# Kernel tuning notes

Hardware: AMD Instinct MI355X
Metric: run time of the kernel (lower is better)

Reference implementation:

```python
import jax, jax.numpy as jnp
import numpy as np

D = 4096       # hidden_size
H = 32         # n_heads (tp_size=1)
DN = 128       # qk_nope_head_dim
DR = 64        # qk_rope_head_dim
DV = 128       # v_head_dim
QL = 1536      # q_lora_rank
KL = 512       # kv_lora_rank
S = 2048       # seqlen, start_pos = 0
EPS = 1e-6
SCALE = (DN + DR) ** -0.5  # softmax_scale (no yarn mscale: seqlen <= original_seq_len)
THETA = 10000.0


def _freqs(seqlen, dim, base=THETA):
    # precompute_freqs_cis without yarn correction (seqlen <= original_seq_len)
    inv = 1.0 / (base ** (np.arange(0, dim, 2, dtype=np.float32) / dim))
    f = np.outer(np.arange(seqlen, dtype=np.float32), inv)  # [S, dim//2]
    return jnp.asarray(np.cos(f)), jnp.asarray(np.sin(f))


def _rmsnorm(x, w):
    return x * jax.lax.rsqrt(jnp.mean(x * x, axis=-1, keepdims=True) + EPS) * w


def _rope(x, cos, sin):
    # x: [S, H, R]; complex rotation on consecutive pairs (view_as_complex semantics)
    S_, H_, R_ = x.shape
    xr = x.reshape(S_, H_, R_ // 2, 2)
    x0, x1 = xr[..., 0], xr[..., 1]
    c = cos[:, None, :]
    s = sin[:, None, :]
    y0 = x0 * c - x1 * s
    y1 = x0 * s + x1 * c
    return jnp.stack([y0, y1], axis=-1).reshape(S_, H_, R_)


def setup_inputs() -> dict:
    key = jax.random.key(0)
    ks = jax.random.split(key, 6)
    std = 0.02
    return {
        "x": jax.random.normal(ks[0], (S, D), jnp.float32),
        "wq_a": jax.random.normal(ks[1], (QL, D), jnp.float32) * std,
        "q_norm_w": jnp.ones((QL,), jnp.float32),
        "wq_b": jax.random.normal(ks[2], (H * (DN + DR), QL), jnp.float32) * std,
        "wkv_a": jax.random.normal(ks[3], (KL + DR, D), jnp.float32) * std,
        "kv_norm_w": jnp.ones((KL,), jnp.float32),
        "wkv_b": jax.random.normal(ks[4], (H * (DN + DV), KL), jnp.float32) * std,
        "wo": jax.random.normal(ks[5], (D, H * DV), jnp.float32) * std,
    }


def reference(x, wq_a, q_norm_w, wq_b, wkv_a, kv_norm_w, wkv_b, wo):
    cos, sin = _freqs(S, DR)

    # q path: low-rank down-proj + RMSNorm + up-proj
    q = _rmsnorm(x @ wq_a.T, q_norm_w) @ wq_b.T          # [S, H*(DN+DR)]
    q = q.reshape(S, H, DN + DR)
    q_nope, q_pe = q[..., :DN], q[..., DN:]
    q_pe = _rope(q_pe, cos, sin)                          # [S, H, DR]

    # kv path: joint latent + rope part
    kv_all = x @ wkv_a.T                                  # [S, KL+DR]
    kv = _rmsnorm(kv_all[:, :KL], kv_norm_w)              # latent kv cache [S, KL]
    k_pe = _rope(kv_all[:, None, KL:], cos, sin)[:, 0, :]  # pe cache [S, DR]

    # absorb k-up-projection into q (einsum 'shd,hdc->shc')
    wkv_b_r = wkv_b.reshape(H, DN + DV, KL)
    q_lat = jnp.einsum("shd,hdc->shc", q_nope, wkv_b_r[:, :DN])  # [S, H, KL]

    scores = (jnp.einsum("shc,tc->sht", q_lat, kv)
              + jnp.einsum("shr,tr->sht", q_pe, k_pe)) * SCALE   # [S, H, T]

    causal = jnp.arange(S)[:, None] >= jnp.arange(S)[None, :]     # [S, T]
    scores = jnp.where(causal[:, None, :], scores, -jnp.inf)
    p = jax.nn.softmax(scores, axis=-1)

    o_lat = jnp.einsum("sht,tc->shc", p, kv)                      # [S, H, KL]
    o = jnp.einsum("shc,hdc->shd", o_lat, wkv_b_r[:, DN:])        # [S, H, DV]
    return o.reshape(S, H * DV) @ wo.T                            # [S, D]
```

## Files before the change

### kernel.cpp

```cpp
#include <hip/hip_runtime.h>
#include <hip/hip_bf16.h>
#include <type_traits>

using bf16 = __hip_bfloat16;
typedef short v8s __attribute__((ext_vector_type(8)));
typedef float v4f __attribute__((ext_vector_type(4)));

#define DEV __device__ __forceinline__

constexpr float SCALE_ = 0.07216878364870322f;

DEV unsigned short bfu(float f) {
  bf16 h = __float2bfloat16(f);
  return __builtin_bit_cast(unsigned short, h);
}
DEV float b2f(short u) {
  unsigned int x = ((unsigned int)(unsigned short)u) << 16;
  return __builtin_bit_cast(float, x);
}

DEV void g2lds16(const void* g, void* l) {
  __builtin_amdgcn_global_load_lds(
      (const __attribute__((address_space(1))) unsigned int*)g,
      (__attribute__((address_space(3))) unsigned int*)l, 16, 0, 0);
}


__global__ void cast_kernel(const float* __restrict__ in, bf16* __restrict__ out, int n4) {
  int i = blockIdx.x * 256 + threadIdx.x;
  int stride = gridDim.x * 256;
  for (; i < n4; i += stride) {
    float4 v = ((const float4*)in)[i];
    ushort4 u;
    u.x = bfu(v.x); u.y = bfu(v.y); u.z = bfu(v.z); u.w = bfu(v.w);
    ((ushort4*)out)[i] = u;
  }
}

__global__ void cast_pad_kernel(const float* __restrict__ in, bf16* __restrict__ out) {
  int i = blockIdx.x * 256 + threadIdx.x;
  float4 v = make_float4(0.f, 0.f, 0.f, 0.f);
  if (i < 589824) v = ((const float4*)in)[i];
  ushort4 u;
  u.x = bfu(v.x); u.y = bfu(v.y); u.z = bfu(v.z); u.w = bfu(v.w);
  ((ushort4*)out)[i] = u;
}

__global__ void wkvbt_kernel(const float* __restrict__ wkvb, bf16* __restrict__ out) {
  int gid = blockIdx.x * 256 + threadIdx.x;
  int c8 = (gid & 63) * 8;
  int d8 = ((gid >> 6) & 15) * 8;
  int h = gid >> 10;
  float4 a[8][2];
#pragma unroll
  for (int r = 0; r < 8; ++r) {
    const float* p = wkvb + ((long)(h * 256 + d8 + r)) * 512 + c8;
    a[r][0] = *(const float4*)p;
    a[r][1] = *(const float4*)(p + 4);
  }
#pragma unroll
  for (int cc = 0; cc < 8; ++cc) {
    v8s o;
#pragma unroll
    for (int r = 0; r < 8; ++r) {
      float f = (cc < 4) ? ((const float*)&a[r][0])[cc] : ((const float*)&a[r][1])[cc - 4];
      o[r] = (short)bfu(f);
    }
    *(v8s*)(out + (long)h * 65536 + (c8 + cc) * 128 + d8) = o;
  }
}

__global__ void wkvbv_kernel(const float* __restrict__ wkvb, bf16* __restrict__ out) {
  int i = blockIdx.x * 256 + threadIdx.x;
  int c4 = i & 127, d = (i >> 7) & 127, h = i >> 14;
  float4 v = *(const float4*)(wkvb + ((long)(h * 256 + 128 + d)) * 512 + c4 * 4);
  ushort4 u;
  u.x = bfu(v.x); u.y = bfu(v.y); u.z = bfu(v.z); u.w = bfu(v.w);
  *(ushort4*)(out + ((long)(h * 128 + d)) * 512 + c4 * 4) = u;
}

__global__ void freqs_kernel(float* __restrict__ cosb, float* __restrict__ sinb) {
  int t = blockIdx.x * 256 + threadIdx.x;
  int s = t >> 5, i = t & 31;
  float inv = powf(10000.0f, -(float)(2 * i) / 64.0f);
  float f = (float)s * inv;
  cosb[t] = cosf(f);
  sinb[t] = sinf(f);
}

__global__ void rmsnorm_bf_kernel(const bf16* __restrict__ in, const float* __restrict__ w,
                                  bf16* __restrict__ out, int L, int ldin, int ldout) {
  int row = blockIdx.x;
  const bf16* x = in + (long)row * ldin;
  int L8 = L >> 3;
  float ss = 0.f;
  for (int i = threadIdx.x; i < L8; i += 256) {
    v8s v = *(const v8s*)(x + i * 8);
#pragma unroll
    for (int j = 0; j < 8; ++j) { float f = b2f(v[j]); ss += f * f; }
  }
#pragma unroll
  for (int d = 1; d < 64; d <<= 1) ss += __shfl_xor(ss, d);
  __shared__ float red[4];
  if ((threadIdx.x & 63) == 0) red[threadIdx.x >> 6] = ss;
  __syncthreads();
  float r = rsqrtf((red[0] + red[1] + red[2] + red[3]) / (float)L + 1e-6f);
  bf16* o = out + (long)row * ldout;
  for (int i = threadIdx.x; i < L8; i += 256) {
    v8s v = *(const v8s*)(x + i * 8);
    v8s u;
#pragma unroll
    for (int j = 0; j < 8; ++j)
      u[j] = (short)bfu(b2f(v[j]) * r * w[i * 8 + j]);
    *(v8s*)(o + i * 8) = u;
  }
}

__global__ void rope_kpe_kernel(const bf16* __restrict__ kvall, const float* __restrict__ cosb,
                                const float* __restrict__ sinb, bf16* __restrict__ keff) {
  int t = blockIdx.x * 256 + threadIdx.x;
  int s = t >> 5, i = t & 31;
  const bf16* p = kvall + (long)s * 640 + 512;
  float x0 = __bfloat162float(p[2 * i]), x1 = __bfloat162float(p[2 * i + 1]);
  float c = cosb[t], sn = sinb[t];
  bf16* o = keff + (long)s * 576 + 512;
  o[2 * i] = __float2bfloat16(x0 * c - x1 * sn);
  o[2 * i + 1] = __float2bfloat16(x0 * sn + x1 * c);
}

__global__ void rope_q_kernel(const bf16* __restrict__ qf, const float* __restrict__ cosb,
                              const float* __restrict__ sinb, bf16* __restrict__ qeff) {
  int t = blockIdx.x * 256 + threadIdx.x;
  int i = t & 31, h = (t >> 5) & 31, s = t >> 10;
  const bf16* p = qf + (long)s * 6144 + h * 192 + 128;
  float x0 = __bfloat162float(p[2 * i]), x1 = __bfloat162float(p[2 * i + 1]);
  float c = cosb[s * 32 + i], sn = sinb[s * 32 + i];
  bf16* o = qeff + (long)s * 18432 + h * 576 + 512;
  o[2 * i] = __float2bfloat16(x0 * c - x1 * sn);
  o[2 * i + 1] = __float2bfloat16(x0 * sn + x1 * c);
}

__global__ void vtrans_kernel(const bf16* __restrict__ keff, bf16* __restrict__ vT) {
  int gid = blockIdx.x * 256 + threadIdx.x;
  int t8 = (gid & 255) * 8, c8 = (gid >> 8) * 8;
  v8s in[8];
#pragma unroll
  for (int r = 0; r < 8; ++r)
    in[r] = *(const v8s*)(keff + (long)(t8 + r) * 576 + c8);
#pragma unroll
  for (int cc = 0; cc < 8; ++cc) {
    v8s o;
#pragma unroll
    for (int r = 0; r < 8; ++r) o[r] = in[r][cc];
    *(v8s*)(vT + (long)(c8 + cc) * 2048 + t8) = o;
  }
}

template <typename OutT>
__global__ __launch_bounds__(256, 3) void gemm_bt(
    const bf16* __restrict__ A, const bf16* __restrict__ B, OutT* __restrict__ C,
    int K, int lda, int ldb, int ldc, long sA, long sB, long sC) {
  __shared__ bf16 lA[4096];
  __shared__ bf16 lB[4096];
  const int tid = threadIdx.x;
  const int lane = tid & 63;
  const int w = tid >> 6, wm = w >> 1, wn = w & 1;
  const int r16 = lane & 15, kg = (lane >> 4) << 3;
  const int arow = tid >> 2, acol = (tid & 3) << 3;
  const bf16* Ab = A + (long)blockIdx.z * sA + (long)blockIdx.y * 128 * lda;
  const bf16* Bb = B + (long)blockIdx.z * sB + (long)blockIdx.x * 128 * ldb;
  v4f acc[4][4] = {};
  for (int k0 = 0; k0 < K; k0 += 32) {
    __syncthreads();
#pragma unroll
    for (int i = 0; i < 2; ++i) {
      g2lds16(Ab + (long)(i * 64 + arow) * lda + (k0 + acol), &lA[i * 2048 + w * 512]);
      g2lds16(Bb + (long)(i * 64 + arow) * ldb + (k0 + acol), &lB[i * 2048 + w * 512]);
    }
    __syncthreads();
    v8s af[4], bfr[4];
#pragma unroll
    for (int mi = 0; mi < 4; ++mi)
      af[mi] = *(const v8s*)&lA[(wm * 64 + mi * 16 + r16) * 32 + kg];
#pragma unroll
    for (int ni = 0; ni < 4; ++ni)
      bfr[ni] = *(const v8s*)&lB[(wn * 64 + ni * 16 + r16) * 32 + kg];
    __builtin_amdgcn_s_setprio(1);
#pragma unroll
    for (int mi = 0; mi < 4; ++mi)
#pragma unroll
      for (int ni = 0; ni < 4; ++ni)
        acc[mi][ni] = __builtin_amdgcn_mfma_f32_16x16x32_bf16(af[mi], bfr[ni], acc[mi][ni], 0, 0, 0);
    __builtin_amdgcn_s_setprio(0);
  }
  OutT* Cb = C + (long)blockIdx.z * sC + (long)(blockIdx.y * 128) * ldc + blockIdx.x * 128;
  const int cr = (lane >> 4) << 2;
#pragma unroll
  for (int mi = 0; mi < 4; ++mi)
#pragma unroll
    for (int ni = 0; ni < 4; ++ni)
#pragma unroll
      for (int j = 0; j < 4; ++j) {
        long idx = (long)(wm * 64 + mi * 16 + cr + j) * ldc + wn * 64 + ni * 16 + r16;
        float v = acc[mi][ni][j];
        if constexpr (std::is_same<OutT, float>::value) Cb[idx] = v;
        else Cb[idx] = __float2bfloat16(v);
      }
}

__device__ const signed char U_QT[24] = {15,15,7,14,14,13,13,6,12,12,11,11,5,10,10,9,9,4,8,8,3,2,1,0};
__device__ const signed char U_HF[24] = {0,1,-1,0,1,0,1,-1,0,1,0,1,-1,0,1,0,1,-1,0,1,-1,-1,-1,-1};

__global__ __launch_bounds__(512, 2) void attn_kernel(
    const bf16* __restrict__ qeff, const bf16* __restrict__ keff,
    const bf16* __restrict__ vT, bf16* __restrict__ olat,
    bf16* __restrict__ P1, float* __restrict__ mlb) {
  __shared__ __align__(16) bf16 kl[32 * 576];
  __shared__ __align__(16) bf16 vl[512 * 32];
  const int tid = threadIdx.x, lane = tid & 63, w = tid >> 6;
  const int r16 = lane & 15, hi = lane >> 4;
  const int kg = hi << 3, cr = hi << 2;
  const int h = blockIdx.x;
  const int u = blockIdx.y;
  const int qt = U_QT[u];
  const int hf = U_HF[u];
  const int nch = 4 * qt + 4;
  const int kc0 = (hf == 1) ? (nch >> 1) : 0;
  const int kc1 = (hf == 0) ? (nch >> 1) : nch;
  const int qrow = qt * 128 + w * 16 + r16;
  const int rb = r16 & 7;

  const long qbase = (long)qrow * 18432 + h * 576;
  v8s qreg[18];
#pragma unroll
  for (int kk = 0; kk < 18; ++kk)
    qreg[kk] = __builtin_nontemporal_load((const v8s*)(qeff + qbase + kk * 32 + kg));

  v4f acc[32] = {};
  float mrow = -1e30f, lrow = 0.f;

  auto stageK = [&](int t0) {
#pragma unroll
    for (int it = 0; it < 5; ++it) {
      int D = it * 512 + tid;
      if (D < 2304) {
        int row = D / 72;
        int gg = D - row * 72;
        int gs = gg ^ (row & 7);
        g2lds16(keff + (long)(t0 + row) * 576 + gs * 8,
                (char*)kl + (it * 512 + w * 64) * 16);
      }
    }
  };
  auto stageV = [&](int t0) {
#pragma unroll
    for (int it = 0; it < 4; ++it) {
      int D = it * 512 + tid;
      int row = D >> 2;
      int s = (D & 3) ^ ((row >> 1) & 3);
      g2lds16(vT + (long)row * 2048 + t0 + s * 8,
              (char*)vl + (it * 512 + w * 64) * 16);
    }
  };

  stageK(kc0 * 32);
  __syncthreads();

  for (int kc = kc0; kc < kc1; ++kc) {
    const int t0 = kc * 32;
    stageV(t0);

    const char* kb = (const char*)kl;
    v4f sf0 = {}, sf1 = {};
    __builtin_amdgcn_s_setprio(1);
#pragma unroll
    for (int kk = 0; kk < 18; ++kk) {
      int so = ((kk * 4 + hi) ^ rb) << 4;
      v8s b0 = *(const v8s*)(kb + r16 * 1152 + so);
      v8s b1 = *(const v8s*)(kb + (16 + r16) * 1152 + so);
      sf0 = __builtin_amdgcn_mfma_f32_16x16x32_bf16(b0, qreg[kk], sf0, 0, 0, 0);
      sf1 = __builtin_amdgcn_mfma_f32_16x16x32_bf16(b1, qreg[kk], sf1, 0, 0, 0);
    }
    __builtin_amdgcn_s_setprio(0);
    float s0[4], s1[4];
#pragma unroll
    for (int j = 0; j < 4; ++j) { s0[j] = sf0[j] * SCALE_; s1[j] = sf1[j] * SCALE_; }
    if (kc >= 4 * qt) {
#pragma unroll
      for (int j = 0; j < 4; ++j) {
        if (t0 + cr + j > qrow) s0[j] = -1e30f;
        if (t0 + 16 + cr + j > qrow) s1[j] = -1e30f;
      }
    }
    float mx = fmaxf(fmaxf(fmaxf(s0[0], s0[1]), fmaxf(s0[2], s0[3])),
                     fmaxf(fmaxf(s1[0], s1[1]), fmaxf(s1[2], s1[3])));
    mx = fmaxf(mx, __shfl_xor(mx, 16));
    mx = fmaxf(mx, __shfl_xor(mx, 32));
    if (!__all(mx <= mrow + 8.0f)) {
      float mn = fmaxf(mrow, mx);
      float alpha = __expf(mrow - mn);
      mrow = mn;
      lrow *= alpha;
      float af0 = __shfl(alpha, cr + 0), af1 = __shfl(alpha, cr + 1);
      float af2 = __shfl(alpha, cr + 2), af3 = __shfl(alpha, cr + 3);
#pragma unroll
      for (int c = 0; c < 32; ++c) {
        acc[c][0] *= af0; acc[c][1] *= af1; acc[c][2] *= af2; acc[c][3] *= af3;
      }
    }
    float p0[4], p1[4];
#pragma unroll
    for (int j = 0; j < 4; ++j) {
      p0[j] = __expf(s0[j] - mrow);
      p1[j] = __expf(s1[j] - mrow);
    }
    float rs = (p0[0] + p0[1]) + (p0[2] + p0[3]) + (p1[0] + p1[1]) + (p1[2] + p1[3]);
    rs += __shfl_xor(rs, 16);
    rs += __shfl_xor(rs, 32);
    lrow += rs;
    int u0 = (int)((unsigned)bfu(p0[0]) | ((unsigned)bfu(p0[1]) << 16));
    int u1 = (int)((unsigned)bfu(p0[2]) | ((unsigned)bfu(p0[3]) << 16));
    int v0 = (int)((unsigned)bfu(p1[0]) | ((unsigned)bfu(p1[1]) << 16));
    int v1 = (int)((unsigned)bfu(p1[2]) | ((unsigned)bfu(p1[3]) << 16));
    const int L1 = r16 + 32 * (hi & 1);
    const int L2 = L1 + 16;
    const bool lo = hi < 2;
    int d0a = __shfl(u0, L1), d0b = __shfl(v0, L1);
    int d1a = __shfl(u1, L1), d1b = __shfl(v1, L1);
    int d2a = __shfl(u0, L2), d2b = __shfl(v0, L2);
    int d3a = __shfl(u1, L2), d3b = __shfl(v1, L2);
    int4 pw = make_int4(lo ? d0a : d0b, lo ? d1a : d1b, lo ? d2a : d2b, lo ? d3a : d3b);
    v8s ap = __builtin_bit_cast(v8s, pw);

    __syncthreads();
    if (kc + 1 < kc1) stageK(t0 + 32);

    __builtin_amdgcn_s_setprio(1);
#pragma unroll
    for (int c = 0; c < 32; ++c) {
      const int vrow = c * 16 + r16;
      const int vsw = (hi ^ ((vrow >> 1) & 3)) << 4;
      v8s bv = *(const v8s*)((const char*)vl + vrow * 64 + vsw);
      acc[c] = __builtin_amdgcn_mfma_f32_16x16x32_bf16(ap, bv, acc[c], 0, 0, 0);
    }
    __builtin_amdgcn_s_setprio(0);
    __syncthreads();
  }
  if (hf < 0) {
    float linv0 = 1.0f / __shfl(lrow, cr + 0);
    float linv1 = 1.0f / __shfl(lrow, cr + 1);
    float linv2 = 1.0f / __shfl(lrow, cr + 2);
    float linv3 = 1.0f / __shfl(lrow, cr + 3);
    const long ob = (long)(qt * 128 + w * 16 + cr) * 16384 + h * 512 + r16;
#pragma unroll
    for (int c = 0; c < 32; ++c) {
      olat[ob + 0 * 16384 + c * 16] = __float2bfloat16(acc[c][0] * linv0);
      olat[ob + 1 * 16384 + c * 16] = __float2bfloat16(acc[c][1] * linv1);
      olat[ob + 2 * 16384 + c * 16] = __float2bfloat16(acc[c][2] * linv2);
      olat[ob + 3 * 16384 + c * 16] = __float2bfloat16(acc[c][3] * linv3);
    }
  } else {
    if (hi == 0) {
      float* mr = mlb + (((qrow - 1024) << 5) + h) * 4 + hf * 2;
      mr[0] = mrow;
      mr[1] = lrow;
    }
    bf16* dst = (hf == 0) ? olat : P1;
    const int rbase = (hf == 0) ? (qt * 128) : (qt * 128 - 1024);
    const long ob = (long)(rbase + w * 16 + cr) * 16384 + h * 512 + r16;
#pragma unroll
    for (int c = 0; c < 32; ++c) {
      dst[ob + 0 * 16384 + c * 16] = __float2bfloat16(acc[c][0]);
      dst[ob + 1 * 16384 + c * 16] = __float2bfloat16(acc[c][1]);
      dst[ob + 2 * 16384 + c * 16] = __float2bfloat16(acc[c][2]);
      dst[ob + 3 * 16384 + c * 16] = __float2bfloat16(acc[c][3]);
    }
  }
}

__global__ void combine_kernel(bf16* __restrict__ olat, const bf16* __restrict__ P1,
                               const float* __restrict__ mlb) {
  int gid = blockIdx.x * 256 + threadIdx.x;
  int cg = gid & 63, h = (gid >> 6) & 31, r = gid >> 11;
  const float* m4 = mlb + ((r << 5) + h) * 4;
  float mA = m4[0], lA = m4[1], mB = m4[2], lB = m4[3];
  float m = fmaxf(mA, mB);
  float sA = __expf(mA - m), sB = __expf(mB - m);
  float inv = 1.0f / (sA * lA + sB * lB);
  sA *= inv; sB *= inv;
  long oa = (long)(1024 + r) * 16384 + h * 512 + cg * 8;
  long ob = (long)r * 16384 + h * 512 + cg * 8;
  v8s a = *(const v8s*)(olat + oa);
  v8s b = *(const v8s*)(P1 + ob);
  v8s o;
#pragma unroll
  for (int j = 0; j < 8; ++j)
    o[j] = (short)bfu(b2f(a[j]) * sA + b2f(b[j]) * sB);
  *(v8s*)(olat + oa) = o;
}


extern "C" void kernel_launch(void* const* d_in, const int* in_sizes, int n_in,
                              void* d_out, int out_size, void* d_ws, size_t ws_size,
                              hipStream_t stream) {
  const float* x = (const float*)d_in[0];
  const float* wq_a = (const float*)d_in[1];
  const float* q_norm_w = (const float*)d_in[2];
  const float* wq_b = (const float*)d_in[3];
  const float* wkv_a = (const float*)d_in[4];
  const float* kv_norm_w = (const float*)d_in[5];
  const float* wkv_b = (const float*)d_in[6];
  const float* wo = (const float*)d_in[7];
  char* ws = (char*)d_ws;

  float* cosb  = (float*)(ws + 0);
  float* sinb  = (float*)(ws + 262144);
  bf16* qeffb  = (bf16*)(ws + 524288);
  bf16* olat   = (bf16*)(ws + 76021760);
  bf16* keff   = (bf16*)(ws + 143130624);
  bf16* vTb    = (bf16*)(ws + 145489920);
  bf16* P1b    = (bf16*)(ws + 147587072);
  float* mlb   = (float*)(ws + 181141504);
  bf16* xb     = (bf16*)(ws + 76021760);
  bf16* wqab   = (bf16*)(ws + 92798976);
  bf16* wkvabp = (bf16*)(ws + 105381888);
  bf16* qa     = (bf16*)(ws + 110624768);
  bf16* kvall  = (bf16*)(ws + 116916224);
  bf16* qan    = (bf16*)(ws + 125829120);
  bf16* wqbb   = (bf16*)(ws + 76021760);
  bf16* qf     = (bf16*)(ws + 94896128);
  bf16* wkvb1t = (bf16*)(ws + 76021760);
  bf16* wkvbv  = (bf16*)(ws + 524288);
  bf16* obuf   = (bf16*)(ws + 4718592);
  bf16* wob    = (bf16*)(ws + 21495808);

  cast_kernel<<<2048, 256, 0, stream>>>(x, xb, 2097152);
  cast_kernel<<<2048, 256, 0, stream>>>(wq_a, wqab, 1572864);
  cast_pad_kernel<<<2560, 256, 0, stream>>>(wkv_a, wkvabp);
  freqs_kernel<<<256, 256, 0, stream>>>(cosb, sinb);

  gemm_bt<bf16><<<dim3(12, 16, 1), 256, 0, stream>>>(xb, wqab, qa, 4096, 4096, 4096, 1536, 0, 0, 0);
  gemm_bt<bf16><<<dim3(5, 16, 1), 256, 0, stream>>>(xb, wkvabp, kvall, 4096, 4096, 4096, 640, 0, 0, 0);

  rmsnorm_bf_kernel<<<2048, 256, 0, stream>>>(qa, q_norm_w, qan, 1536, 1536, 1536);
  rmsnorm_bf_kernel<<<2048, 256, 0, stream>>>(kvall, kv_norm_w, keff, 512, 640, 576);
  rope_kpe_kernel<<<256, 256, 0, stream>>>(kvall, cosb, sinb, keff);
  vtrans_kernel<<<64, 256, 0, stream>>>(keff, vTb);

  cast_kernel<<<2048, 256, 0, stream>>>(wq_b, wqbb, 2359296);
  gemm_bt<bf16><<<dim3(48, 16, 1), 256, 0, stream>>>(qan, wqbb, qf, 1536, 1536, 1536, 6144, 0, 0, 0);

  rope_q_kernel<<<8192, 256, 0, stream>>>(qf, cosb, sinb, qeffb);
  wkvbt_kernel<<<128, 256, 0, stream>>>(wkv_b, wkvb1t);
  gemm_bt<bf16><<<dim3(4, 16, 32), 256, 0, stream>>>(qf, wkvb1t, qeffb,
      128, 6144, 128, 18432, 192L, 65536L, 576L);

  attn_kernel<<<dim3(32, 24), 512, 0, stream>>>(qeffb, keff, vTb, olat, P1b, mlb);
  combine_kernel<<<8192, 256, 0, stream>>>(olat, P1b, mlb);

  wkvbv_kernel<<<2048, 256, 0, stream>>>(wkv_b, wkvbv);
  gemm_bt<bf16><<<dim3(1, 16, 32), 256, 0, stream>>>(olat, wkvbv, obuf,
      512, 16384, 512, 4096, 512L, 65536L, 128L);

  cast_kernel<<<2048, 256, 0, stream>>>(wo, wob, 4194304);
  gemm_bt<float><<<dim3(32, 16, 1), 256, 0, stream>>>(obuf, wob, (float*)d_out,
      4096, 4096, 4096, 4096, 0, 0, 0);
}
```

Measured before the change: 707.5 us.

## Merge q/kv down-projection GEMMs and add a specialized K=128 absorb GEMM

The x@wq_a and x@wkv_a projections become one GEMM writing a combined [S, 2176] buffer. This relies on the bf16 copies of wq_a and the padded wkv_a sitting next to each other in the workspace. The RMSNorm and k_pe RoPE kernels now read from this combined buffer with a stride of 2176. A new gemm_k128 kernel handles the q_nope x wkv_b absorption: it loads the whole K=128 tile into LDS in one pass and runs no k-loop pipeline. The aim is to cut launch overhead and improve CU fill from the merged GEMM, and to drop loop overhead from the small-K batched GEMM.

New measurement: 645.6 us, median of 2. -8.7%, faster.

```diff
diff --git a/kernel.cpp b/kernel.cpp
--- a/kernel.cpp
+++ b/kernel.cpp
@@ -116,11 +116,11 @@
   }
 }
 
-__global__ void rope_kpe_kernel(const bf16* __restrict__ kvall, const float* __restrict__ cosb,
+__global__ void rope_kpe_kernel(const bf16* __restrict__ qakv, const float* __restrict__ cosb,
                                 const float* __restrict__ sinb, bf16* __restrict__ keff) {
   int t = blockIdx.x * 256 + threadIdx.x;
   int s = t >> 5, i = t & 31;
-  const bf16* p = kvall + (long)s * 640 + 512;
+  const bf16* p = qakv + (long)s * 2176 + 2048;
   float x0 = __bfloat162float(p[2 * i]), x1 = __bfloat162float(p[2 * i + 1]);
   float c = cosb[t], sn = sinb[t];
   bf16* o = keff + (long)s * 576 + 512;
@@ -205,6 +205,61 @@
         float v = acc[mi][ni][j];
         if constexpr (std::is_same<OutT, float>::value) Cb[idx] = v;
         else Cb[idx] = __float2bfloat16(v);
+      }
+}
+
+__global__ __launch_bounds__(256, 2) void gemm_k128(
+    const bf16* __restrict__ A, const bf16* __restrict__ B, bf16* __restrict__ C,
+    int lda, int ldb, int ldc, long sA, long sB, long sC) {
+  __shared__ bf16 lA[16384];
+  __shared__ bf16 lB[16384];
+  const int tid = threadIdx.x;
+  const int lane = tid & 63;
+  const int w = tid >> 6, wm = w >> 1, wn = w & 1;
+  const int r16 = lane & 15, hi = lane >> 4;
+  const bf16* Ab = A + (long)blockIdx.z * sA + (long)blockIdx.y * 128 * lda;
+  const bf16* Bb = B + (long)blockIdx.z * sB + (long)blockIdx.x * 128 * ldb;
+#pragma unroll
+  for (int it = 0; it < 8; ++it) {
+    int D = it * 256 + tid;
+    int row = D >> 4, sl = D & 15;
+    int gs = sl ^ (row & 7);
+    g2lds16(Ab + (long)row * lda + gs * 8, (char*)lA + (it * 256 + w * 64) * 16);
+    g2lds16(Bb + (long)row * ldb + gs * 8, (char*)lB + (it * 256 + w * 64) * 16);
+  }
+  __syncthreads();
+  v4f acc[4][4] = {};
+#pragma unroll
+  for (int kk = 0; kk < 4; ++kk) {
+    v8s af[4], bfr[4];
+#pragma unroll
+    for (int mi = 0; mi < 4; ++mi) {
+      int r = wm * 64 + mi * 16 + r16;
+      af[mi] = *(const v8s*)((const char*)lA + (r * 16 + ((kk * 4 + hi) ^ (r & 7))) * 16);
+    }
+#pragma unroll
+    for (int ni = 0; ni < 4; ++ni) {
+      int r = wn * 64 + ni * 16 + r16;
+      bfr[ni] = *(const v8s*)((const char*)lB + (r * 16 + ((kk * 4 + hi) ^ (r & 7))) * 16);
+    }
+    __builtin_amdgcn_s_setprio(1);
+#pragma unroll
+    for (int mi = 0; mi < 4; ++mi)
+#pragma unroll
+      for (int ni = 0; ni < 4; ++ni)
+        acc[mi][ni] = __builtin_amdgcn_mfma_f32_16x16x32_bf16(af[mi], bfr[ni], acc[mi][ni], 0, 0, 0);
+    __builtin_amdgcn_s_setprio(0);
+  }
+  bf16* Cb = C + (long)blockIdx.z * sC + (long)(blockIdx.y * 128) * ldc + blockIdx.x * 128;
+  const int cr = hi << 2;
+#pragma unroll
+  for (int mi = 0; mi < 4; ++mi)
+#pragma unroll
+    for (int ni = 0; ni < 4; ++ni)
+#pragma unroll
+      for (int j = 0; j < 4; ++j) {
+        long idx = (long)(wm * 64 + mi * 16 + cr + j) * ldc + wn * 64 + ni * 16 + r16;
+        Cb[idx] = __float2bfloat16(acc[mi][ni][j]);
       }
 }
 
@@ -424,8 +479,7 @@
   bf16* xb     = (bf16*)(ws + 76021760);
   bf16* wqab   = (bf16*)(ws + 92798976);
   bf16* wkvabp = (bf16*)(ws + 105381888);
-  bf16* qa     = (bf16*)(ws + 110624768);
-  bf16* kvall  = (bf16*)(ws + 116916224);
+  bf16* qakv   = (bf16*)(ws + 110624768);
   bf16* qan    = (bf16*)(ws + 125829120);
   bf16* wqbb   = (bf16*)(ws + 76021760);
   bf16* qf     = (bf16*)(ws + 94896128);
@@ -439,12 +493,11 @@
   cast_pad_kernel<<<2560, 256, 0, stream>>>(wkv_a, wkvabp);
   freqs_kernel<<<256, 256, 0, stream>>>(cosb, sinb);
 
-  gemm_bt<bf16><<<dim3(12, 16, 1), 256, 0, stream>>>(xb, wqab, qa, 4096, 4096, 4096, 1536, 0, 0, 0);
-  gemm_bt<bf16><<<dim3(5, 16, 1), 256, 0, stream>>>(xb, wkvabp, kvall, 4096, 4096, 4096, 640, 0, 0, 0);
-
-  rmsnorm_bf_kernel<<<2048, 256, 0, stream>>>(qa, q_norm_w, qan, 1536, 1536, 1536);
-  rmsnorm_bf_kernel<<<2048, 256, 0, stream>>>(kvall, kv_norm_w, keff, 512, 640, 576);
-  rope_kpe_kernel<<<256, 256, 0, stream>>>(kvall, cosb, sinb, keff);
+  gemm_bt<bf16><<<dim3(17, 16, 1), 256, 0, stream>>>(xb, wqab, qakv, 4096, 4096, 4096, 2176, 0, 0, 0);
+
+  rmsnorm_bf_kernel<<<2048, 256, 0, stream>>>(qakv, q_norm_w, qan, 1536, 2176, 1536);
+  rmsnorm_bf_kernel<<<2048, 256, 0, stream>>>(qakv + 1536, kv_norm_w, keff, 512, 2176, 576);
+  rope_kpe_kernel<<<256, 256, 0, stream>>>(qakv, cosb, sinb, keff);
   vtrans_kernel<<<64, 256, 0, stream>>>(keff, vTb);
 
   cast_kernel<<<2048, 256, 0, stream>>>(wq_b, wqbb, 2359296);
@@ -452,8 +505,8 @@
 
   rope_q_kernel<<<8192, 256, 0, stream>>>(qf, cosb, sinb, qeffb);
   wkvbt_kernel<<<128, 256, 0, stream>>>(wkv_b, wkvb1t);
-  gemm_bt<bf16><<<dim3(4, 16, 32), 256, 0, stream>>>(qf, wkvb1t, qeffb,
-      128, 6144, 128, 18432, 192L, 65536L, 576L);
+  gemm_k128<<<dim3(4, 16, 32), 256, 0, stream>>>(qf, wkvb1t, qeffb,
+      6144, 128, 18432, 192L, 65536L, 576L);
 
   attn_kernel<<<dim3(32, 24), 512, 0, stream>>>(qeffb, keff, vTb, olat, P1b, mlb);
   combine_kernel<<<8192, 256, 0, stream>>>(olat, P1b, mlb);
```
